# Performance work log

Hardware: AMD Instinct MI355X
Metric: run time of the kernel (lower is better)

## Reference

```python
import jax, jax.numpy as jnp
import numpy as np


def _per_sample_ce(logits, targets):
    # -log_softmax(logits)[i, targets[i]]  -> shape [N]
    logp = jax.nn.log_softmax(logits, axis=-1)
    return -jnp.take_along_axis(logp, targets[:, None], axis=-1)[:, 0]


def setup_inputs() -> dict:
    key = jax.random.key(0)
    k1, k2, k3 = jax.random.split(key, 3)
    N, C = 65536, 1000
    y_1 = jax.random.normal(k1, (N, C), dtype=jnp.float32)
    y_2 = jax.random.normal(k2, (N, C), dtype=jnp.float32)
    targets = jax.random.randint(k3, (N,), 0, C, dtype=jnp.int64)
    num_keep = 45875  # int(0.7 * N), static for jit
    return {"y_1": y_1, "y_2": y_2, "targets": targets, "num_keep": num_keep}


def reference(y_1, y_2, targets, num_keep):
    loss_1 = _per_sample_ce(y_1, targets)          # [N]
    loss_2 = _per_sample_ce(y_2, targets)          # [N]
    # small-loss selection: indices of the num_keep smallest per-sample losses
    ind_1_update = jnp.argsort(loss_1)[:num_keep]  # selected by net 1
    ind_2_update = jnp.argsort(loss_2)[:num_keep]  # selected by net 2
    # cross-update: each net trains on the peer's selected samples
    loss_1_update = _per_sample_ce(y_1[ind_2_update], targets[ind_2_update])
    loss_2_update = _per_sample_ce(y_2[ind_1_update], targets[ind_1_update])
    # size_average=True -> means
    return (loss_1_update.mean(), loss_2_update.mean(),
            loss_1.mean(), loss_2.mean())
```

## Files before the change

### kernel.cpp

```cpp
#include <hip/hip_runtime.h>
#include <math.h>

#define MAXT 2048

__device__ __forceinline__ unsigned keyOf(float f) {
  unsigned b = __float_as_uint(f);
  return b ^ ((b & 0x80000000u) ? 0xFFFFFFFFu : 0x80000000u);
}

__device__ __forceinline__ float waveSum(float v) {
#pragma unroll
  for (int o = 32; o >= 1; o >>= 1) v += __shfl_xor(v, o);
  return v;
}

__device__ __forceinline__ void selectStep(const unsigned* __restrict__ h,
                                           int per, unsigned rank,
                                           unsigned* sc, unsigned* res) {
  int t = threadIdx.x;
  unsigned local[8];
  unsigned s = 0;
  for (int j = 0; j < per; ++j) { local[j] = h[t * per + j]; s += local[j]; }
  sc[t] = s;
  __syncthreads();
  for (int off = 1; off < 256; off <<= 1) {
    unsigned v = (t >= off) ? sc[t - off] : 0u;
    __syncthreads();
    sc[t] += v;
    __syncthreads();
  }
  unsigned incl = sc[t], excl = incl - s;
  if (excl < rank && rank <= incl) {
    unsigned cum = excl;
    for (int j = 0; j < per; ++j) {
      if (cum + local[j] >= rank) {
        res[0] = (unsigned)(t * per + j);
        res[1] = rank - cum;
        break;
      }
      cum += local[j];
    }
  }
  __syncthreads();
}

__device__ __forceinline__ void ceFinish(int row, int t, int lane,
                                         float4 a, float4 b, float4 c,
                                         float4 d, float* __restrict__ L) {
  const float L2E = 1.4426950408889634f;
  const float LN2 = 0.6931471805599453f;
  int vecIdx = t >> 2;
  int grp = vecIdx >> 6, srcLane = vecIdx & 63, comp = t & 3;
  float4 sel = (grp == 0) ? a : (grp == 1) ? b : (grp == 2) ? c : d;
  float cand = (comp == 0) ? sel.x : (comp == 1) ? sel.y
             : (comp == 2) ? sel.z : sel.w;
  float xt = __shfl(cand, srcLane);
#define E_(v) exp2f((v) * L2E)
  float s = (((E_(a.x) + E_(a.y)) + (E_(a.z) + E_(a.w))) +
             ((E_(b.x) + E_(b.y)) + (E_(b.z) + E_(b.w)))) +
            (((E_(c.x) + E_(c.y)) + (E_(c.z) + E_(c.w))) +
             ((E_(d.x) + E_(d.y)) + (E_(d.z) + E_(d.w))));
#undef E_
  s = waveSum(s);
  if (lane == 0) L[row] = log2f(s) * LN2 - xt;
}

__global__ __launch_bounds__(256) void ce_kernel(
    const float* __restrict__ y1, const float* __restrict__ y2,
    const int* __restrict__ tgt,
    float* __restrict__ l1, float* __restrict__ l2,
    unsigned* __restrict__ zeroBase, int zeroCount, int N) {
  if (blockIdx.x == 0) {
    for (int j = threadIdx.x; j < zeroCount; j += 256) zeroBase[j] = 0u;
  }
  int wid = threadIdx.x >> 6, lane = threadIdx.x & 63;
  int w = blockIdx.x * 4 + wid;
  int nWaves = gridDim.x * 4;
  int net = w & 1;
  int r = w >> 1;
  int rstride = nWaves >> 1;
  if (r >= N) return;
  const float* Y = net ? y2 : y1;
  float* L = net ? l2 : l1;
  const float4 negInf = make_float4(-INFINITY, -INFINITY, -INFINITY, -INFINITY);
  int dOff = (lane < 58) ? (lane + 192) : 249;

  const float4* p = (const float4*)(Y + (size_t)r * 1000);
  int ct = tgt[r];
  float4 a = p[lane], b = p[lane + 64], c = p[lane + 128], d = p[dOff];
  if (lane >= 58) d = negInf;

  for (int rn = r + rstride; rn < N; rn += rstride) {
    const float4* q = (const float4*)(Y + (size_t)rn * 1000);
    int nt = tgt[rn];
    float4 na = q[lane], nb = q[lane + 64], nc = q[lane + 128], nd = q[dOff];
    if (lane >= 58) nd = negInf;
    ceFinish(r, ct, lane, a, b, c, d, L);
    a = na; b = nb; c = nc; d = nd; ct = nt; r = rn;
  }
  ceFinish(r, ct, lane, a, b, c, d, L);
}

__global__ __launch_bounds__(256) void histA_kernel(
    const float* __restrict__ l1, const float* __restrict__ l2,
    unsigned* __restrict__ hA1, unsigned* __restrict__ hA2, int N) {
  __shared__ unsigned lh[2][2048];
  int t = threadIdx.x;
  for (int j = t; j < 2048; j += 256) { lh[0][j] = 0u; lh[1][j] = 0u; }
  __syncthreads();
  for (int i = blockIdx.x * blockDim.x + t; i < N;
       i += gridDim.x * blockDim.x) {
    atomicAdd(&lh[0][keyOf(l1[i]) >> 21], 1u);
    atomicAdd(&lh[1][keyOf(l2[i]) >> 21], 1u);
  }
  __syncthreads();
  for (int j = t; j < 2048; j += 256) {
    unsigned v0 = lh[0][j], v1 = lh[1][j];
    if (v0) atomicAdd(&hA1[j], v0);
    if (v1) atomicAdd(&hA2[j], v1);
  }
}

__global__ __launch_bounds__(256) void histB_kernel(
    const float* __restrict__ l1, const float* __restrict__ l2,
    const unsigned* __restrict__ hA1, const unsigned* __restrict__ hA2,
    unsigned* __restrict__ hB1, unsigned* __restrict__ hB2,
    const int* __restrict__ numKeep, int N) {
  __shared__ unsigned sc[256];
  __shared__ unsigned resA1[2], resA2[2];
  unsigned k0 = (unsigned)(*numKeep);
  selectStep(hA1, 8, k0, sc, resA1);
  selectStep(hA2, 8, k0, sc, resA2);
  unsigned a1 = resA1[0], a2 = resA2[0];
  for (int i = blockIdx.x * blockDim.x + threadIdx.x; i < N;
       i += gridDim.x * blockDim.x) {
    unsigned k1 = keyOf(l1[i]);
    if ((k1 >> 21) == a1) atomicAdd(&hB1[(k1 >> 10) & 2047u], 1u);
    unsigned k2 = keyOf(l2[i]);
    if ((k2 >> 21) == a2) atomicAdd(&hB2[(k2 >> 10) & 2047u], 1u);
  }
}

__global__ __launch_bounds__(256) void partial_kernel(
    const float* __restrict__ l1, const float* __restrict__ l2,
    const unsigned* __restrict__ hA1, const unsigned* __restrict__ hA2,
    const unsigned* __restrict__ hB1, const unsigned* __restrict__ hB2,
    const int* __restrict__ numKeep, unsigned* __restrict__ tc,
    unsigned* __restrict__ done,
    int* __restrict__ tIdx1, unsigned* __restrict__ tKey1, float* __restrict__ tVal1,
    int* __restrict__ tIdx2, unsigned* __restrict__ tKey2, float* __restrict__ tVal2,
    float* __restrict__ partials, float* __restrict__ out, int N) {
  __shared__ unsigned sc[256];
  __shared__ unsigned rA1[2], rA2[2], rB1[2], rB2[2];
  unsigned k0 = (unsigned)(*numKeep);
  selectStep(hA1, 8, k0, sc, rA1);
  selectStep(hA2, 8, k0, sc, rA2);
  selectStep(hB1, 8, rA1[1], sc, rB1);
  selectStep(hB2, 8, rA2[1], sc, rB2);
  unsigned P1 = (rA1[0] << 11) | rB1[0];
  unsigned P2 = (rA2[0] << 11) | rB2[0];
  float s0 = 0.f, s1 = 0.f, s2 = 0.f, s3 = 0.f;
  for (int i = blockIdx.x * blockDim.x + threadIdx.x; i < N;
       i += gridDim.x * blockDim.x) {
    float f1 = l1[i], f2 = l2[i];
    unsigned k1 = keyOf(f1), k2 = keyOf(f2);
    unsigned q1 = k1 >> 10, q2 = k2 >> 10;
    if (q2 < P2) {
      s0 += f1;
    } else if (q2 == P2) {
      unsigned p = atomicAdd(&tc[1], 1u);
      if (p < MAXT) { tIdx2[p] = i; tKey2[p] = k2; tVal2[p] = f1; }
    }
    if (q1 < P1) {
      s1 += f2;
    } else if (q1 == P1) {
      unsigned p = atomicAdd(&tc[0], 1u);
      if (p < MAXT) { tIdx1[p] = i; tKey1[p] = k1; tVal1[p] = f2; }
    }
    s2 += f1;
    s3 += f2;
  }
  s0 = waveSum(s0); s1 = waveSum(s1); s2 = waveSum(s2); s3 = waveSum(s3);
  __shared__ float red[4][4];
  int wid = threadIdx.x >> 6, lane = threadIdx.x & 63;
  if (lane == 0) {
    red[wid][0] = s0; red[wid][1] = s1; red[wid][2] = s2; red[wid][3] = s3;
  }
  __syncthreads();
  if (threadIdx.x == 0) {
    for (int q = 0; q < 4; ++q)
      partials[blockIdx.x * 4 + q] =
          red[0][q] + red[1][q] + red[2][q] + red[3][q];
  }
  __shared__ unsigned amLast;
  __threadfence();
  if (threadIdx.x == 0)
    amLast = (atomicAdd(done, 1u) == (unsigned)(gridDim.x - 1)) ? 1u : 0u;
  __syncthreads();
  if (!amLast) return;
  __threadfence();
  int t = threadIdx.x;
  float u0 = 0.f, u1 = 0.f, u2 = 0.f, u3 = 0.f;
  for (int j = t; j < (int)gridDim.x; j += 256) {
    u0 += partials[j * 4 + 0];
    u1 += partials[j * 4 + 1];
    u2 += partials[j * 4 + 2];
    u3 += partials[j * 4 + 3];
  }
  u0 = waveSum(u0); u1 = waveSum(u1); u2 = waveSum(u2); u3 = waveSum(u3);
  __syncthreads();
  if (lane == 0) {
    red[wid][0] = u0; red[wid][1] = u1; red[wid][2] = u2; red[wid][3] = u3;
  }
  __shared__ float slots[MAXT];
  __shared__ float tieSum[2];
  unsigned needArr[2] = {rB1[1], rB2[1]};
  for (int a = 0; a < 2; ++a) {
    const int* ti = a ? tIdx2 : tIdx1;
    const unsigned* tk = a ? tKey2 : tKey1;
    const float* tv = a ? tVal2 : tVal1;
    int T = min((int)tc[a], MAXT);
    int need = min((int)needArr[a], T);
    __syncthreads();
    for (int j = t; j < T; j += 256) {
      int idx = ti[j];
      unsigned kj = tk[j];
      int rk = 0;
      for (int m = 0; m < T; ++m) {
        unsigned km = tk[m];
        rk += (km < kj || (km == kj && ti[m] < idx)) ? 1 : 0;
      }
      if (rk < need) slots[rk] = tv[j];
    }
    __syncthreads();
    if (t == 0) {
      float s = 0.f;
      for (int j = 0; j < need; ++j) s += slots[j];
      tieSum[a] = s;
    }
  }
  __syncthreads();
  if (t == 0) {
    float a0 = red[0][0] + red[1][0] + red[2][0] + red[3][0] + tieSum[1];
    float a1 = red[0][1] + red[1][1] + red[2][1] + red[3][1] + tieSum[0];
    float a2 = red[0][2] + red[1][2] + red[2][2] + red[3][2];
    float a3 = red[0][3] + red[1][3] + red[2][3] + red[3][3];
    float k = (float)k0;
    out[0] = a0 / k;
    out[1] = a1 / k;
    out[2] = a2 / (float)N;
    out[3] = a3 / (float)N;
  }
}

extern "C" void kernel_launch(void* const* d_in, const int* in_sizes, int n_in,
                              void* d_out, int out_size, void* d_ws,
                              size_t ws_size, hipStream_t stream) {
  const float* y1 = (const float*)d_in[0];
  const float* y2 = (const float*)d_in[1];
  const int* tgt = (const int*)d_in[2];
  const int* numKeep = (const int*)d_in[3];
  int N = in_sizes[2];
  float* out = (float*)d_out;

  float* l1 = (float*)d_ws;
  float* l2 = l1 + N;
  unsigned* hA1 = (unsigned*)(l2 + N);
  unsigned* hA2 = hA1 + 2048;
  unsigned* hB1 = hA2 + 2048;
  unsigned* hB2 = hB1 + 2048;
  unsigned* tc = hB2 + 2048;
  unsigned* done = tc + 2;
  int* tIdx1 = (int*)(done + 1);
  unsigned* tKey1 = (unsigned*)(tIdx1 + MAXT);
  float* tVal1 = (float*)(tKey1 + MAXT);
  int* tIdx2 = (int*)(tVal1 + MAXT);
  unsigned* tKey2 = (unsigned*)(tIdx2 + MAXT);
  float* tVal2 = (float*)(tKey2 + MAXT);
  float* partials = (float*)(tVal2 + MAXT);

  ce_kernel<<<2048, 256, 0, stream>>>(y1, y2, tgt, l1, l2, hA1,
                                      4 * 2048 + 3, N);
  histA_kernel<<<256, 256, 0, stream>>>(l1, l2, hA1, hA2, N);
  histB_kernel<<<256, 256, 0, stream>>>(l1, l2, hA1, hA2, hB1, hB2, numKeep, N);
  partial_kernel<<<256, 256, 0, stream>>>(l1, l2, hA1, hA2, hB1, hB2, numKeep,
                                          tc, done, tIdx1, tKey1, tVal1, tIdx2,
                                          tKey2, tVal2, partials, out, N);
}
```

Measured before the change: 149.9 us.

## Replace persistent prefetching CE kernel with one-row-per-wave grid and max-stabilized softmax

The persistent grid-stride CE kernel with software prefetch is replaced by a launch of N/4 blocks where each wave handles one row for both networks, reusing the target lookup. A wave-wide max reduction is added so the log-sum-exp is numerically stabilized. Zeroing of the histogram workspace moves into a separate single-block init kernel. This trades explicit prefetch pipelining for occupancy-driven latency hiding, and adds an extra max reduction, extra shuffles and an extra kernel launch.

```diff
diff --git a/kernel.cpp b/kernel.cpp
--- a/kernel.cpp
+++ b/kernel.cpp
@@ -44,61 +44,58 @@
   __syncthreads();
 }
 
-__device__ __forceinline__ void ceFinish(int row, int t, int lane,
-                                         float4 a, float4 b, float4 c,
-                                         float4 d, float* __restrict__ L) {
-  const float L2E = 1.4426950408889634f;
-  const float LN2 = 0.6931471805599453f;
-  int vecIdx = t >> 2;
-  int grp = vecIdx >> 6, srcLane = vecIdx & 63, comp = t & 3;
-  float4 sel = (grp == 0) ? a : (grp == 1) ? b : (grp == 2) ? c : d;
-  float cand = (comp == 0) ? sel.x : (comp == 1) ? sel.y
-             : (comp == 2) ? sel.z : sel.w;
-  float xt = __shfl(cand, srcLane);
-#define E_(v) exp2f((v) * L2E)
-  float s = (((E_(a.x) + E_(a.y)) + (E_(a.z) + E_(a.w))) +
-             ((E_(b.x) + E_(b.y)) + (E_(b.z) + E_(b.w)))) +
-            (((E_(c.x) + E_(c.y)) + (E_(c.z) + E_(c.w))) +
-             ((E_(d.x) + E_(d.y)) + (E_(d.z) + E_(d.w))));
-#undef E_
-  s = waveSum(s);
-  if (lane == 0) L[row] = log2f(s) * LN2 - xt;
+__global__ __launch_bounds__(256) void init_kernel(unsigned* __restrict__ z,
+                                                   int count) {
+  for (int j = threadIdx.x; j < count; j += 256) z[j] = 0u;
 }
 
 __global__ __launch_bounds__(256) void ce_kernel(
     const float* __restrict__ y1, const float* __restrict__ y2,
     const int* __restrict__ tgt,
-    float* __restrict__ l1, float* __restrict__ l2,
-    unsigned* __restrict__ zeroBase, int zeroCount, int N) {
-  if (blockIdx.x == 0) {
-    for (int j = threadIdx.x; j < zeroCount; j += 256) zeroBase[j] = 0u;
-  }
+    float* __restrict__ l1, float* __restrict__ l2, int N) {
+  const float L2E = 1.4426950408889634f;
+  const float LN2 = 0.6931471805599453f;
   int wid = threadIdx.x >> 6, lane = threadIdx.x & 63;
-  int w = blockIdx.x * 4 + wid;
-  int nWaves = gridDim.x * 4;
-  int net = w & 1;
-  int r = w >> 1;
-  int rstride = nWaves >> 1;
-  if (r >= N) return;
-  const float* Y = net ? y2 : y1;
-  float* L = net ? l2 : l1;
-  const float4 negInf = make_float4(-INFINITY, -INFINITY, -INFINITY, -INFINITY);
-  int dOff = (lane < 58) ? (lane + 192) : 249;
-
-  const float4* p = (const float4*)(Y + (size_t)r * 1000);
-  int ct = tgt[r];
-  float4 a = p[lane], b = p[lane + 64], c = p[lane + 128], d = p[dOff];
-  if (lane >= 58) d = negInf;
-
-  for (int rn = r + rstride; rn < N; rn += rstride) {
-    const float4* q = (const float4*)(Y + (size_t)rn * 1000);
-    int nt = tgt[rn];
-    float4 na = q[lane], nb = q[lane + 64], nc = q[lane + 128], nd = q[dOff];
-    if (lane >= 58) nd = negInf;
-    ceFinish(r, ct, lane, a, b, c, d, L);
-    a = na; b = nb; c = nc; d = nd; ct = nt; r = rn;
-  }
-  ceFinish(r, ct, lane, a, b, c, d, L);
+  int row = blockIdx.x * 4 + wid;
+  if (row >= N) return;
+  int t = tgt[row];
+  int vecIdx = t >> 2;
+  int grp = vecIdx >> 6;
+  int srcLane = vecIdx & 63;
+  int comp = t & 3;
+#pragma unroll
+  for (int which = 0; which < 2; ++which) {
+    const float* y = which ? y2 : y1;
+    const float4* rp = (const float4*)(y + (size_t)row * 1000);
+    float4 a = rp[lane];
+    float4 b = rp[lane + 64];
+    float4 c = rp[lane + 128];
+    float4 d = make_float4(-INFINITY, -INFINITY, -INFINITY, -INFINITY);
+    if (lane + 192 < 250) d = rp[lane + 192];
+    float4 sel = (grp == 0) ? a : (grp == 1) ? b : (grp == 2) ? c : d;
+    float cand = (comp == 0) ? sel.x : (comp == 1) ? sel.y
+               : (comp == 2) ? sel.z : sel.w;
+    float xt = __shfl(cand, srcLane);
+    float m = fmaxf(fmaxf(fmaxf(a.x, a.y), fmaxf(a.z, a.w)),
+                    fmaxf(fmaxf(b.x, b.y), fmaxf(b.z, b.w)));
+    m = fmaxf(m, fmaxf(fmaxf(c.x, c.y), fmaxf(c.z, c.w)));
+    m = fmaxf(m, fmaxf(fmaxf(d.x, d.y), fmaxf(d.z, d.w)));
+#pragma unroll
+    for (int o = 32; o >= 1; o >>= 1) m = fmaxf(m, __shfl_xor(m, o));
+    float s = exp2f((a.x - m) * L2E) + exp2f((a.y - m) * L2E) +
+              exp2f((a.z - m) * L2E) + exp2f((a.w - m) * L2E) +
+              exp2f((b.x - m) * L2E) + exp2f((b.y - m) * L2E) +
+              exp2f((b.z - m) * L2E) + exp2f((b.w - m) * L2E) +
+              exp2f((c.x - m) * L2E) + exp2f((c.y - m) * L2E) +
+              exp2f((c.z - m) * L2E) + exp2f((c.w - m) * L2E) +
+              exp2f((d.x - m) * L2E) + exp2f((d.y - m) * L2E) +
+              exp2f((d.z - m) * L2E) + exp2f((d.w - m) * L2E);
+    s = waveSum(s);
+    if (lane == 0) {
+      float loss = log2f(s) * LN2 + m - xt;
+      (which ? l2 : l1)[row] = loss;
+    }
+  }
 }
 
 __global__ __launch_bounds__(256) void histA_kernel(
@@ -279,8 +276,8 @@
   float* tVal2 = (float*)(tKey2 + MAXT);
   float* partials = (float*)(tVal2 + MAXT);
 
-  ce_kernel<<<2048, 256, 0, stream>>>(y1, y2, tgt, l1, l2, hA1,
-                                      4 * 2048 + 3, N);
+  init_kernel<<<1, 256, 0, stream>>>(hA1, 4 * 2048 + 3);
+  ce_kernel<<<(N + 3) / 4, 256, 0, stream>>>(y1, y2, tgt, l1, l2, N);
   histA_kernel<<<256, 256, 0, stream>>>(l1, l2, hA1, hA2, N);
   histB_kernel<<<256, 256, 0, stream>>>(l1, l2, hA1, hA2, hB1, hB2, numKeep, N);
   partial_kernel<<<256, 256, 0, stream>>>(l1, l2, hA1, hA2, hB1, hB2, numKeep,
```

Result: no change. 152.8 us (+2.0%).
